# Kernel tuning notes

Measured on AMD Instinct MI355X. Metric: run time of the kernel, lower is better.

The kernel has to match this reference:

```python
import jax, jax.numpy as jnp
import numpy as np

N, E, F, HID, PC, HEADS = 100000, 1600000, 128, 128, 16, 4
RATIO = 0.8
NEG_SLOPE = 0.2
BIG_NEG = -1e9


def setup_inputs() -> dict:
    ks = jax.random.split(jax.random.key(0), 20)
    def g(k, shape, fan):
        return jax.random.normal(k, shape, jnp.float32) / np.float32(np.sqrt(fan))
    return {
        "x": jax.random.normal(ks[0], (N, F), jnp.float32),
        "edge_index": jax.random.randint(ks[1], (2, E), 0, N, dtype=jnp.int32),
        "edge_attr": jax.random.uniform(ks[2], (E, 1), dtype=jnp.float32),
        "W1": g(ks[3], (F, PC), F),
        "att_src1": g(ks[4], (HEADS, PC // HEADS), PC // HEADS),
        "att_dst1": g(ks[5], (HEADS, PC // HEADS), PC // HEADS),
        "We1": g(ks[6], (1, PC), 1),
        "att_edge1": g(ks[7], (HEADS, PC // HEADS), PC // HEADS),
        "b1": jnp.zeros((PC,), jnp.float32),
        "Wrel": g(ks[8], (PC, 1), PC),
        "brel": jnp.zeros((1,), jnp.float32),
        "Wroot": g(ks[9], (PC, 1), PC),
        "W2": g(ks[10], (PC, HID), PC),
        "att_src2": g(ks[11], (1, HID), HID),
        "att_dst2": g(ks[12], (1, HID), HID),
        "We2": g(ks[13], (1, HID), 1),
        "att_edge2": g(ks[14], (1, HID), HID),
        "b2": jnp.zeros((HID,), jnp.float32),
        "Wg": g(ks[15], (HID, 1), HID),
        "bg": jnp.zeros((1,), jnp.float32),
    }


def gat_conv(h_in, src, dst, e_attr, W, a_s, a_d, We, a_e, b, num_nodes, mask=None):
    """PyG GATConv (add_self_loops=False, eval-mode so dropout is identity)."""
    H, D = a_s.shape
    h = (h_in @ W).reshape(-1, H, D)                      # [N,H,D]
    al_s = jnp.einsum('nhd,hd->nh', h, a_s)               # alpha contribution of source
    al_d = jnp.einsum('nhd,hd->nh', h, a_d)               # alpha contribution of dest
    he = (e_attr @ We).reshape(-1, H, D)                  # [E,H,D] edge features
    al_e = jnp.einsum('ehd,hd->eh', he, a_e)              # [E,H]
    logits = jax.nn.leaky_relu(al_s[src] + al_d[dst] + al_e, NEG_SLOPE)  # [E,H]
    if mask is not None:
        logits = jnp.where(mask[:, None], logits, BIG_NEG)
    # segment softmax over incoming edges of each destination node
    m = jnp.maximum(jax.ops.segment_max(logits, dst, num_segments=num_nodes), BIG_NEG)
    num = jnp.exp(logits - m[dst])
    if mask is not None:
        num = jnp.where(mask[:, None], num, 0.0)
    den = jax.ops.segment_sum(num, dst, num_segments=num_nodes)
    coef = num / jnp.maximum(den[dst], 1e-16)             # [E,H]
    out = jax.ops.segment_sum(coef[:, :, None] * h[src], dst, num_segments=num_nodes)
    return out.reshape(num_nodes, H * D) + b


def _forward(x, edge_attr, W1, att_src1, att_dst1, We1, att_edge1, b1,
             Wrel, brel, Wroot, W2, att_src2, att_dst2, We2, att_edge2, b2,
             Wg, bg, edge_index):
    n = x.shape[0]
    src, dst = edge_index[0], edge_index[1]
    h1 = jax.nn.relu(gat_conv(x, src, dst, edge_attr, W1, att_src1, att_dst1, We1, att_edge1, b1, n))
    # --- SAGPooling: GraphConv score -> tanh -> top-k -> masked subgraph (n > node_threshold always) ---
    agg = jax.ops.segment_sum(h1[src], dst, num_segments=n)           # neighbor sum
    score = (agg @ Wrel + brel + h1 @ Wroot).reshape(-1)              # GraphConv(16 -> 1)
    k = int(np.ceil(RATIO * n))                                       # static
    vals, perm = jax.lax.top_k(score, k)
    new_idx = jnp.full((n,), -1, dtype=jnp.int32).at[perm].set(jnp.arange(k, dtype=jnp.int32))
    src_n, dst_n = new_idx[src], new_idx[dst]
    emask = (src_n >= 0) & (dst_n >= 0)                               # edges with both ends kept
    src2 = jnp.where(emask, src_n, 0)
    dst2 = jnp.where(emask, dst_n, 0)
    x2 = h1[perm] * jnp.tanh(vals)[:, None]                           # gate kept nodes
    h2 = jax.nn.relu(gat_conv(x2, src2, dst2, edge_attr, W2, att_src2, att_dst2, We2, att_edge2, b2, k, mask=emask))
    # --- AttentionalAggregation + MaxAggregation over the single graph (index = zeros) ---
    gate = jax.nn.softmax(h2 @ Wg + bg, axis=0)                       # [k,1]
    att = (gate * h2).sum(axis=0, keepdims=True)                      # [1,HID]
    mx = h2.max(axis=0, keepdims=True)                                # [1,HID]
    return jnp.concatenate([att, mx], axis=1)                         # [1,2*HID]


def reference(x, edge_index, edge_attr, W1, att_src1, att_dst1, We1, att_edge1, b1,
              Wrel, brel, Wroot, W2, att_src2, att_dst2, We2, att_edge2, b2, Wg, bg):
    return _forward(x, edge_attr, W1, att_src1, att_dst1, We1, att_edge1, b1,
                    Wrel, brel, Wroot, W2, att_src2, att_dst2, We2, att_edge2, b2,
                    Wg, bg, edge_index)
```

## Files before the change

kernel.cpp:

```cpp
#include <hip/hip_runtime.h>
#include <hip/hip_bf16.h>

#define Nn 100000
#define Ee 1600000
#define Kk 80000
#define NB ((Nn + 255) / 256)
#define NBK 196
#define CHK 8192
#define G2B 2048

typedef unsigned int uint;
typedef unsigned short ushort;

struct Scal {
    uint prefix, remaining;
    float c1[4];
    float c2;
};

__device__ __forceinline__ uint f2ord(float f) {
    uint b = __float_as_uint(f);
    return (b & 0x80000000u) ? ~b : (b | 0x80000000u);
}
__device__ __forceinline__ float lrelu(float v) { return v > 0.f ? v : 0.2f * v; }
__device__ __forceinline__ float2 bf2f2(uint u) {
    return make_float2(__uint_as_float(u << 16), __uint_as_float(u & 0xFFFF0000u));
}

__global__ __launch_bounds__(256) void initK(uint* bcnt, uint* hist, Scal* sc,
                                             const float* We1, const float* ae1,
                                             const float* We2, const float* ae2) {
    int i = blockIdx.x * 256 + threadIdx.x;
    if (i < NBK) bcnt[i] = 0u;
    if (i < 256) hist[i] = 0u;
    if (i == 0) {
        sc->prefix = 0u; sc->remaining = Kk;
        for (int h = 0; h < 4; h++) {
            float s = 0.f;
            for (int d = 0; d < 4; d++) s += We1[h * 4 + d] * ae1[h * 4 + d];
            sc->c1[h] = s;
        }
        float s2 = 0.f;
        for (int d = 0; d < 128; d++) s2 += We2[d] * ae2[d];
        sc->c2 = s2;
    }
}

__global__ __launch_bounds__(256) void nodeL1(const float* __restrict__ x,
                                              const float* __restrict__ W1,
                                              const float* __restrict__ as1,
                                              const float* __restrict__ ad1,
                                              float* __restrict__ hpre,
                                              float* __restrict__ alS1,
                                              float* __restrict__ alD1) {
    __shared__ float Ws[128 * 16];
    __shared__ float s_as[16], s_ad[16];
    for (int i = threadIdx.x; i < 2048; i += 256) Ws[i] = W1[i];
    if (threadIdx.x < 16) { s_as[threadIdx.x] = as1[threadIdx.x]; s_ad[threadIdx.x] = ad1[threadIdx.x]; }
    __syncthreads();
    int n = blockIdx.x * 256 + threadIdx.x;
    if (n >= Nn) return;
    float acc[16];
#pragma unroll
    for (int j = 0; j < 16; j++) acc[j] = 0.f;
    const float4* xr = (const float4*)(x + (size_t)n * 128);
    for (int t4 = 0; t4 < 32; t4++) {
        float4 xv = xr[t4];
#pragma unroll
        for (int j = 0; j < 16; j++) {
            acc[j] += xv.x * Ws[(t4 * 4 + 0) * 16 + j];
            acc[j] += xv.y * Ws[(t4 * 4 + 1) * 16 + j];
            acc[j] += xv.z * Ws[(t4 * 4 + 2) * 16 + j];
            acc[j] += xv.w * Ws[(t4 * 4 + 3) * 16 + j];
        }
    }
    float* hp = hpre + (size_t)n * 16;
#pragma unroll
    for (int j = 0; j < 16; j++) hp[j] = acc[j];
#pragma unroll
    for (int h = 0; h < 4; h++) {
        float s = 0.f, d = 0.f;
#pragma unroll
        for (int q = 0; q < 4; q++) {
            s += acc[h * 4 + q] * s_as[h * 4 + q];
            d += acc[h * 4 + q] * s_ad[h * 4 + q];
        }
        alS1[n * 4 + h] = s;
        alD1[n * 4 + h] = d;
    }
}

__global__ __launch_bounds__(256) void bucketCnt(const int* __restrict__ ei, uint* __restrict__ bcnt) {
    __shared__ uint h[NBK];
    if (threadIdx.x < NBK) h[threadIdx.x] = 0u;
    __syncthreads();
    for (int e = blockIdx.x * 256 + threadIdx.x; e < Ee; e += gridDim.x * 256)
        atomicAdd(&h[((uint)ei[Ee + e]) >> 9], 1u);
    __syncthreads();
    if (threadIdx.x < NBK && h[threadIdx.x]) atomicAdd(&bcnt[threadIdx.x], h[threadIdx.x]);
}

__global__ __launch_bounds__(256) void scanBk(const uint* __restrict__ bcnt, uint* __restrict__ boff,
                                              uint* __restrict__ gcur) {
    __shared__ uint s[256];
    int t = threadIdx.x;
    uint v = (t < NBK) ? bcnt[t] : 0u;
    s[t] = v;
    __syncthreads();
    for (int off = 1; off < 256; off <<= 1) {
        uint u = (t >= off) ? s[t - off] : 0u;
        __syncthreads();
        s[t] += u;
        __syncthreads();
    }
    if (t < NBK) { boff[t] = s[t] - v; gcur[t] = 0u; }
    if (t == 0) boff[NBK] = Ee;
}

__global__ __launch_bounds__(256) void binScat(const int* __restrict__ ei, const float* __restrict__ ea,
                                               const uint* __restrict__ boff, uint* __restrict__ gcur,
                                               uint2* __restrict__ bsE, ushort* __restrict__ bsD) {
    __shared__ uint h[NBK], base[NBK], h2[NBK];
    int t = threadIdx.x;
    if (t < NBK) h[t] = 0u;
    __syncthreads();
    int estart = blockIdx.x * CHK;
    int eend = min(Ee, estart + CHK);
    for (int e = estart + t; e < eend; e += 256)
        atomicAdd(&h[((uint)ei[Ee + e]) >> 9], 1u);
    __syncthreads();
    if (t < NBK) { base[t] = atomicAdd(&gcur[t], h[t]); h2[t] = 0u; }
    __syncthreads();
    for (int e = estart + t; e < eend; e += 256) {
        uint d = (uint)ei[Ee + e];
        uint b = d >> 9;
        uint r = atomicAdd(&h2[b], 1u);
        uint pos = boff[b] + base[b] + r;
        bsE[pos] = make_uint2((uint)ei[e], __float_as_uint(ea[e]));
        bsD[pos] = (ushort)(d & 511u);
    }
}

__global__ __launch_bounds__(256) void rankPlace(const uint* __restrict__ boff, const uint2* __restrict__ bsE,
                                                 const ushort* __restrict__ bsD,
                                                 uint2* __restrict__ csr_p8, uint* __restrict__ rowstart) {
    __shared__ uint ldeg[512];
    __shared__ uint lscan[512];
    __shared__ uint ps[256];
    int b = blockIdx.x, t = threadIdx.x;
    ldeg[t] = 0u; ldeg[t + 256] = 0u;
    __syncthreads();
    uint r0 = boff[b], r1 = boff[b + 1];
    for (uint i = r0 + t; i < r1; i += 256)
        atomicAdd(&ldeg[bsD[i]], 1u);
    __syncthreads();
    uint pv = ldeg[2 * t] + ldeg[2 * t + 1];
    ps[t] = pv;
    __syncthreads();
    for (int off = 1; off < 256; off <<= 1) {
        uint u = (t >= off) ? ps[t - off] : 0u;
        __syncthreads();
        ps[t] += u;
        __syncthreads();
    }
    uint pbase = ps[t] - pv;
    lscan[2 * t] = pbase;
    lscan[2 * t + 1] = pbase + ldeg[2 * t];
    __syncthreads();
    uint bb = boff[b];
    int nd = b * 512 + t;
    if (nd < Nn) rowstart[nd] = bb + lscan[t];
    nd = b * 512 + 256 + t;
    if (nd < Nn) rowstart[nd] = bb + lscan[256 + t];
    if (b == 0 && t == 0) rowstart[Nn] = Ee;
    ldeg[t] = 0u; ldeg[t + 256] = 0u;
    __syncthreads();
    for (uint i = r0 + t; i < r1; i += 256) {
        ushort dl = bsD[i];
        uint r = atomicAdd(&ldeg[dl], 1u);
        csr_p8[bb + lscan[dl] + r] = bsE[i];
    }
}

__global__ __launch_bounds__(256) void gather1f(const uint2* __restrict__ csr_p8,
                                                const uint* __restrict__ rowstart,
                                                const float* __restrict__ alS1, const float* __restrict__ alD1,
                                                const float* __restrict__ hpre, const Scal* __restrict__ scc,
                                                const float* __restrict__ b1, const float* __restrict__ Wrel,
                                                const float* __restrict__ Wroot,
                                                float* __restrict__ h1, float* __restrict__ p,
                                                float* __restrict__ q) {
    int tid = blockIdx.x * 256 + threadIdx.x;
    if (tid >= Nn * 4) return;
    int d = tid >> 2, h = tid & 3;
    uint r0 = rowstart[d], r1 = rowstart[d + 1];
    float ad = alD1[tid];
    float c1h = scc->c1[h];
    float den = 0.f;
    float4 acc = {0.f, 0.f, 0.f, 0.f};
#pragma unroll 8
    for (uint i = r0; i < r1; i++) {
        uint2 p8 = csr_p8[i];
        int s = (int)p8.x;
        float e = __expf(lrelu(alS1[s * 4 + h] + __uint_as_float(p8.y) * c1h + ad));
        float4 hv = *(const float4*)(hpre + (size_t)s * 16 + h * 4);
        den += e;
        acc.x += e * hv.x; acc.y += e * hv.y;
        acc.z += e * hv.z; acc.w += e * hv.w;
    }
    float inv = 1.f / fmaxf(den, 1e-16f);
    float4 o;
    o.x = fmaxf(acc.x * inv + b1[h * 4 + 0], 0.f);
    o.y = fmaxf(acc.y * inv + b1[h * 4 + 1], 0.f);
    o.z = fmaxf(acc.z * inv + b1[h * 4 + 2], 0.f);
    o.w = fmaxf(acc.w * inv + b1[h * 4 + 3], 0.f);
    *(float4*)(h1 + (size_t)d * 16 + h * 4) = o;
    float pp = o.x * Wrel[h * 4 + 0] + o.y * Wrel[h * 4 + 1] + o.z * Wrel[h * 4 + 2] + o.w * Wrel[h * 4 + 3];
    float qq = o.x * Wroot[h * 4 + 0] + o.y * Wroot[h * 4 + 1] + o.z * Wroot[h * 4 + 2] + o.w * Wroot[h * 4 + 3];
    pp += __shfl_xor(pp, 1); pp += __shfl_xor(pp, 2);
    qq += __shfl_xor(qq, 1); qq += __shfl_xor(qq, 2);
    if (h == 0) { p[d] = pp; q[d] = qq; }
}

__global__ __launch_bounds__(256) void scoreH(const uint2* __restrict__ csr_p8, const uint* __restrict__ rowstart,
                                              const float* __restrict__ p, const float* __restrict__ q,
                                              const float* __restrict__ brel,
                                              float* __restrict__ score, uint* __restrict__ dkey,
                                              uint* __restrict__ hist) {
    __shared__ uint lh[256];
    lh[threadIdx.x] = 0u;
    __syncthreads();
    int d = blockIdx.x * 256 + threadIdx.x;
    if (d < Nn) {
        uint r0 = rowstart[d], r1 = rowstart[d + 1];
        float s = brel[0] + q[d];
#pragma unroll 8
        for (uint i = r0; i < r1; i++) s += p[(int)csr_p8[i].x];
        score[d] = s;
        uint k = ~f2ord(s);
        dkey[d] = k;
        atomicAdd(&lh[k >> 24], 1u);
    }
    __syncthreads();
    if (lh[threadIdx.x]) atomicAdd(&hist[threadIdx.x], lh[threadIdx.x]);
}

__global__ __launch_bounds__(256) void histK(const uint* __restrict__ dkey, const Scal* __restrict__ sc,
                                             uint* __restrict__ hist, int shift) {
    __shared__ uint lh[256];
    lh[threadIdx.x] = 0u;
    __syncthreads();
    int i = blockIdx.x * 256 + threadIdx.x;
    if (i < Nn) {
        uint d = dkey[i];
        if ((d >> (shift + 8)) == sc->prefix) atomicAdd(&lh[(d >> shift) & 255u], 1u);
    }
    __syncthreads();
    if (lh[threadIdx.x]) atomicAdd(&hist[threadIdx.x], lh[threadIdx.x]);
}

__global__ __launch_bounds__(256) void selP(Scal* sc, uint* hist) {
    __shared__ uint s[256];
    int t = threadIdx.x;
    uint c = hist[t];
    s[t] = c;
    __syncthreads();
    for (int off = 1; off < 256; off <<= 1) {
        uint v = (t >= off) ? s[t - off] : 0u;
        __syncthreads();
        s[t] += v;
        __syncthreads();
    }
    uint rem = sc->remaining;
    uint cum = s[t];
    uint cumex = cum - c;
    if (cum >= rem && cumex < rem) {
        sc->remaining = rem - cumex;
        sc->prefix = (sc->prefix << 8) | (uint)t;
    }
    hist[t] = 0u;
}

__global__ __launch_bounds__(256) void eqCnt(const uint* __restrict__ dkey, const Scal* __restrict__ sc,
                                             uint* __restrict__ blkEq) {
    int i = blockIdx.x * 256 + threadIdx.x;
    uint ut = sc->prefix;
    bool eq = (i < Nn) && (dkey[i] == ut);
    __shared__ uint se[4];
    unsigned long long be = __ballot(eq);
    int lane = threadIdx.x & 63, w = threadIdx.x >> 6;
    if (lane == 0) se[w] = (uint)__popcll(be);
    __syncthreads();
    if (threadIdx.x == 0) blkEq[blockIdx.x] = se[0] + se[1] + se[2] + se[3];
}

__global__ __launch_bounds__(512) void prefE(const uint* __restrict__ blkEq, uint* __restrict__ eqPref) {
    __shared__ uint se[512];
    int t = threadIdx.x;
    uint e = (t < NB) ? blkEq[t] : 0u;
    se[t] = e;
    __syncthreads();
    for (int off = 1; off < 512; off <<= 1) {
        uint v1 = (t >= off) ? se[t - off] : 0u;
        __syncthreads();
        se[t] += v1;
        __syncthreads();
    }
    if (t < NB) eqPref[t] = se[t] - e;
}

__global__ __launch_bounds__(256) void keptK(const uint* __restrict__ dkey, const Scal* __restrict__ sc,
                                             const uint* __restrict__ eqPref, int* __restrict__ kept) {
    int i = blockIdx.x * 256 + threadIdx.x;
    uint ut = sc->prefix, needEq = sc->remaining;
    bool inr = i < Nn;
    uint d = inr ? dkey[i] : 0xFFFFFFFFu;
    bool isLt = inr && (d < ut);
    bool isEq = inr && (d == ut);
    __shared__ uint wcnt[4];
    unsigned long long mask = __ballot(isEq);
    int lane = threadIdx.x & 63, w = threadIdx.x >> 6;
    uint lanePre = (uint)__popcll(mask & ((1ull << lane) - 1ull));
    if (lane == 0) wcnt[w] = (uint)__popcll(mask);
    __syncthreads();
    uint wo = 0;
    for (int qq = 0; qq < 4; qq++) if (qq < w) wo += wcnt[qq];
    uint rank = eqPref[blockIdx.x] + wo + lanePre;
    if (inr) kept[i] = (isLt || (isEq && rank < needEq)) ? 1 : 0;
}

__global__ __launch_bounds__(256) void nodeL2(const float* __restrict__ h1, const float* __restrict__ score,
                                              const int* __restrict__ kept, const float* __restrict__ W2,
                                              const float* __restrict__ as2, const float* __restrict__ ad2,
                                              __hip_bfloat162* __restrict__ h2b, float* __restrict__ alS2k,
                                              float* __restrict__ alD2) {
    __shared__ float Ws[16 * 128];
    for (int i = threadIdx.x; i < 2048; i += 256) Ws[i] = W2[i];
    __syncthreads();
    int wid = (blockIdx.x * 256 + threadIdx.x) >> 6;
    int lane = threadIdx.x & 63;
    if (wid >= Nn) return;
    int n = wid;
    if (!kept[n]) { if (lane == 0) alS2k[n] = -1e30f; return; }
    float t = tanhf(score[n]);
    float x2[16];
    const float* hr = h1 + (size_t)n * 16;
#pragma unroll
    for (int j = 0; j < 16; j++) x2[j] = hr[j] * t;
    int d0 = 2 * lane, d1 = 2 * lane + 1;
    float a0 = 0.f, a1 = 0.f;
    const float2* Wv = (const float2*)Ws;
#pragma unroll
    for (int j = 0; j < 16; j++) {
        float2 wv = Wv[j * 64 + lane];
        a0 += x2[j] * wv.x;
        a1 += x2[j] * wv.y;
    }
    __hip_bfloat162 hb;
    hb.x = __float2bfloat16(a0);
    hb.y = __float2bfloat16(a1);
    h2b[(size_t)n * 64 + lane] = hb;
    float s = a0 * as2[d0] + a1 * as2[d1];
    float dd = a0 * ad2[d0] + a1 * ad2[d1];
#pragma unroll
    for (int off = 32; off; off >>= 1) { s += __shfl_xor(s, off); dd += __shfl_xor(dd, off); }
    if (lane == 0) { alS2k[n] = s; alD2[n] = dd; }
}

__global__ __launch_bounds__(256) void gather2g(const uint2* __restrict__ csr_p8,
                                                const uint* __restrict__ rowstart,
                                                const float* __restrict__ alS2k, const float* __restrict__ alD2,
                                                const Scal* __restrict__ scc,
                                                const __hip_bfloat162* __restrict__ h2b, const float* __restrict__ b2,
                                                const float* __restrict__ Wg, const float* __restrict__ bg,
                                                float* __restrict__ pacc, float* __restrict__ pmx,
                                                float* __restrict__ pden) {
    __shared__ float sAtt[4][16][8];
    __shared__ float sMx[4][16][8];
    __shared__ float sDen[4];
    int w = threadIdx.x >> 6, lane = threadIdx.x & 63;
    int g = lane >> 4, t = lane & 15;
    float4 b2a = ((const float4*)b2)[t * 2], b2b = ((const float4*)b2)[t * 2 + 1];
    float4 wga = ((const float4*)Wg)[t * 2], wgb = ((const float4*)Wg)[t * 2 + 1];
    float bg0 = bg[0];
    float c2 = scc->c2;
    const uint* h2u = (const uint*)h2b;
    float att[8], mx8[8], denP = 0.f;
#pragma unroll
    for (int j = 0; j < 8; j++) { att[j] = 0.f; mx8[j] = 0.f; }
    for (int n = blockIdx.x * 4 + w; n < Nn; n += G2B * 4) {
        float sk = alS2k[n];
        if (sk <= -1e29f) continue;
        float ad = alD2[n];
        uint r0 = rowstart[n];
        uint len = rowstart[n + 1] - r0;
        float den = 0.f;
        float acc[8];
#pragma unroll
        for (int d = 0; d < 8; d++) acc[d] = 0.f;
#pragma unroll 4
        for (uint base = 0; base < len; base += 4) {
            uint off = base + (uint)g;
            bool act = off < len;
            uint sidx = act ? (r0 + off) : (r0 + len - 1);
            uint2 p8 = csr_p8[sidx];
            int s = (int)p8.x;
            float pv = alS2k[s] + __uint_as_float(p8.y) * c2;
            pv = act ? pv : -1e30f;
            float c = __expf(lrelu(pv + ad));
            uint4 hv = *(const uint4*)(h2u + (size_t)s * 64 + t * 4);
            den += c;
            float2 f;
            f = bf2f2(hv.x); acc[0] += c * f.x; acc[1] += c * f.y;
            f = bf2f2(hv.y); acc[2] += c * f.x; acc[3] += c * f.y;
            f = bf2f2(hv.z); acc[4] += c * f.x; acc[5] += c * f.y;
            f = bf2f2(hv.w); acc[6] += c * f.x; acc[7] += c * f.y;
        }
#pragma unroll
        for (int d = 0; d < 8; d++) {
            acc[d] += __shfl_xor(acc[d], 16);
            acc[d] += __shfl_xor(acc[d], 32);
        }
        den += __shfl_xor(den, 16);
        den += __shfl_xor(den, 32);
        float inv = 1.f / fmaxf(den, 1e-16f);
        float o[8];
        o[0] = fmaxf(acc[0] * inv + b2a.x, 0.f);
        o[1] = fmaxf(acc[1] * inv + b2a.y, 0.f);
        o[2] = fmaxf(acc[2] * inv + b2a.z, 0.f);
        o[3] = fmaxf(acc[3] * inv + b2a.w, 0.f);
        o[4] = fmaxf(acc[4] * inv + b2b.x, 0.f);
        o[5] = fmaxf(acc[5] * inv + b2b.y, 0.f);
        o[6] = fmaxf(acc[6] * inv + b2b.z, 0.f);
        o[7] = fmaxf(acc[7] * inv + b2b.w, 0.f);
        float gp = o[0] * wga.x + o[1] * wga.y + o[2] * wga.z + o[3] * wga.w +
                   o[4] * wgb.x + o[5] * wgb.y + o[6] * wgb.z + o[7] * wgb.w;
#pragma unroll
        for (int off = 8; off; off >>= 1) gp += __shfl_xor(gp, off);
        float e = __expf(gp + bg0);
        denP += e;
#pragma unroll
        for (int j = 0; j < 8; j++) {
            att[j] += e * o[j];
            mx8[j] = fmaxf(mx8[j], o[j]);
        }
    }
    if (g == 0) {
#pragma unroll
        for (int j = 0; j < 8; j++) { sAtt[w][t][j] = att[j]; sMx[w][t][j] = mx8[j]; }
    }
    if (lane == 0) sDen[w] = denP;
    __syncthreads();
    int tid = threadIdx.x;
    if (tid < 128) {
        int tt = tid >> 3, j = tid & 7;
        float a = sAtt[0][tt][j] + sAtt[1][tt][j] + sAtt[2][tt][j] + sAtt[3][tt][j];
        float m = fmaxf(fmaxf(sMx[0][tt][j], sMx[1][tt][j]), fmaxf(sMx[2][tt][j], sMx[3][tt][j]));
        pacc[(size_t)blockIdx.x * 128 + tid] = a;
        pmx[(size_t)blockIdx.x * 128 + tid] = m;
    }
    if (tid == 0) pden[blockIdx.x] = sDen[0] + sDen[1] + sDen[2] + sDen[3];
}

__global__ __launch_bounds__(256) void gateOut(const float* __restrict__ pacc, const float* __restrict__ pmx,
                                               const float* __restrict__ pden, float* __restrict__ out) {
    __shared__ float r[256];
    __shared__ float rd[256];
    int b = blockIdx.x, tid = threadIdx.x;
    float a = 0.f, m = 0.f, dsum = 0.f;
    for (int i = tid; i < G2B; i += 256) {
        a += pacc[(size_t)i * 128 + b];
        m = fmaxf(m, pmx[(size_t)i * 128 + b]);
        dsum += pden[i];
    }
    r[tid] = a; rd[tid] = dsum;
    __syncthreads();
    for (int off = 128; off; off >>= 1) {
        if (tid < off) { r[tid] += r[tid + off]; rd[tid] += rd[tid + off]; }
        __syncthreads();
    }
    float asum = r[0], deng = rd[0];
    __syncthreads();
    r[tid] = m;
    __syncthreads();
    for (int off = 128; off; off >>= 1) {
        if (tid < off) r[tid] = fmaxf(r[tid], r[tid + off]);
        __syncthreads();
    }
    if (tid == 0) {
        out[b] = asum / deng;
        out[128 + b] = r[0];
    }
}

extern "C" void kernel_launch(void* const* d_in, const int* in_sizes, int n_in,
                              void* d_out, int out_size, void* d_ws, size_t ws_size,
                              hipStream_t stream) {
    const float* x = (const float*)d_in[0];
    const int* ei = (const int*)d_in[1];
    const float* ea = (const float*)d_in[2];
    const float* W1 = (const float*)d_in[3];
    const float* as1 = (const float*)d_in[4];
    const float* ad1 = (const float*)d_in[5];
    const float* We1 = (const float*)d_in[6];
    const float* ae1 = (const float*)d_in[7];
    const float* b1 = (const float*)d_in[8];
    const float* Wrel = (const float*)d_in[9];
    const float* brel = (const float*)d_in[10];
    const float* Wroot = (const float*)d_in[11];
    const float* W2 = (const float*)d_in[12];
    const float* as2 = (const float*)d_in[13];
    const float* ad2 = (const float*)d_in[14];
    const float* We2 = (const float*)d_in[15];
    const float* ae2 = (const float*)d_in[16];
    const float* b2 = (const float*)d_in[17];
    const float* Wg = (const float*)d_in[18];
    const float* bg = (const float*)d_in[19];
    float* out = (float*)d_out;

    float* base = (float*)d_ws;
    size_t o = 0;
    auto alloc = [&](size_t nf) { float* p2 = base + o; o += nf; return p2; };
    uint2* bsE = (uint2*)alloc((size_t)Ee * 2);
    ushort* bsD = (ushort*)alloc((size_t)Ee / 2);
    uint2* csr_p8 = (uint2*)alloc((size_t)Ee * 2);
    __hip_bfloat162* h2b = (__hip_bfloat162*)alloc((size_t)Nn * 64);
    float* hpre = alloc((size_t)Nn * 16);
    float* h1 = alloc((size_t)Nn * 16);
    float* pacc = alloc((size_t)G2B * 128);
    float* pmx = alloc((size_t)G2B * 128);
    float* pden = alloc(G2B);
    float* alS1 = alloc((size_t)Nn * 4);
    float* alD1 = alloc((size_t)Nn * 4);
    float* p = alloc(Nn);
    float* q = alloc(Nn);
    float* score = alloc(Nn);
    uint* dkey = (uint*)alloc(Nn);
    int* kept = (int*)alloc(Nn);
    float* alS2k = alloc(Nn);
    float* alD2 = alloc(Nn);
    uint* rowstart = (uint*)alloc(Nn + 1);
    uint* hist = (uint*)alloc(256);
    uint* blkEq = (uint*)alloc(NB);
    uint* eqPref = (uint*)alloc(NB);
    uint* bcnt = (uint*)alloc(NBK);
    uint* boff = (uint*)alloc(NBK + 1);
    uint* gcur = (uint*)alloc(NBK);
    Scal* sc = (Scal*)alloc(64);

    auto cdiv = [](long a, long b) { return (int)((a + b - 1) / b); };

    initK<<<NB, 256, 0, stream>>>(bcnt, hist, sc, We1, ae1, We2, ae2);
    nodeL1<<<NB, 256, 0, stream>>>(x, W1, as1, ad1, hpre, alS1, alD1);
    bucketCnt<<<512, 256, 0, stream>>>(ei, bcnt);
    scanBk<<<1, 256, 0, stream>>>(bcnt, boff, gcur);
    binScat<<<cdiv(Ee, CHK), 256, 0, stream>>>(ei, ea, boff, gcur, bsE, bsD);
    rankPlace<<<NBK, 256, 0, stream>>>(boff, bsE, bsD, csr_p8, rowstart);
    gather1f<<<cdiv((long)Nn * 4, 256), 256, 0, stream>>>(csr_p8, rowstart, alS1, alD1, hpre, sc,
                                                          b1, Wrel, Wroot, h1, p, q);
    scoreH<<<NB, 256, 0, stream>>>(csr_p8, rowstart, p, q, brel, score, dkey, hist);
    selP<<<1, 256, 0, stream>>>(sc, hist);
    for (int shift = 16; shift >= 0; shift -= 8) {
        histK<<<NB, 256, 0, stream>>>(dkey, sc, hist, shift);
        selP<<<1, 256, 0, stream>>>(sc, hist);
    }
    eqCnt<<<NB, 256, 0, stream>>>(dkey, sc, blkEq);
    prefE<<<1, 512, 0, stream>>>(blkEq, eqPref);
    keptK<<<NB, 256, 0, stream>>>(dkey, sc, eqPref, kept);
    nodeL2<<<cdiv(Nn, 4), 256, 0, stream>>>(h1, score, kept, W2, as2, ad2, h2b, alS2k, alD2);
    gather2g<<<G2B, 256, 0, stream>>>(csr_p8, rowstart, alS2k, alD2, sc,
                                      h2b, b2, Wg, bg, pacc, pmx, pden);
    gateOut<<<128, 256, 0, stream>>>(pacc, pmx, pden, out);
}
```

Before: 328.0 us.

## Store layer-1 node features as bf16 and use finer 256-node CSR buckets

The projected layer-1 node features are now written as packed bf16 instead of fp32, which halves the bytes fetched per edge in the gather1f aggregation. The CSR build is reorganised around 256-node buckets (391 of them) with smaller per-block edge chunks. This gives more blocks for binScat and rankPlace and lighter per-block local scans. The bf16 storage costs precision in the layer-1 aggregation, which feeds the top-k score selection and could change which nodes are kept.

Measured after the change: 335.4 us. +2.3%, slower.

```diff
diff --git a/kernel.cpp b/kernel.cpp
--- a/kernel.cpp
+++ b/kernel.cpp
@@ -5,8 +5,8 @@
 #define Ee 1600000
 #define Kk 80000
 #define NB ((Nn + 255) / 256)
-#define NBK 196
-#define CHK 8192
+#define NBK 391
+#define CHK 2048
 #define G2B 2048
 
 typedef unsigned int uint;
@@ -25,6 +25,12 @@
 __device__ __forceinline__ float lrelu(float v) { return v > 0.f ? v : 0.2f * v; }
 __device__ __forceinline__ float2 bf2f2(uint u) {
     return make_float2(__uint_as_float(u << 16), __uint_as_float(u & 0xFFFF0000u));
+}
+__device__ __forceinline__ uint f2bf2(float a, float b) {
+    __hip_bfloat162 h;
+    h.x = __float2bfloat16(a);
+    h.y = __float2bfloat16(b);
+    return *(uint*)&h;
 }
 
 __global__ __launch_bounds__(256) void initK(uint* bcnt, uint* hist, Scal* sc,
@@ -50,7 +56,7 @@
                                               const float* __restrict__ W1,
                                               const float* __restrict__ as1,
                                               const float* __restrict__ ad1,
-                                              float* __restrict__ hpre,
+                                              uint* __restrict__ hpreB,
                                               float* __restrict__ alS1,
                                               float* __restrict__ alD1) {
     __shared__ float Ws[128 * 16];
@@ -74,9 +80,12 @@
             acc[j] += xv.w * Ws[(t4 * 4 + 3) * 16 + j];
         }
     }
-    float* hp = hpre + (size_t)n * 16;
-#pragma unroll
-    for (int j = 0; j < 16; j++) hp[j] = acc[j];
+    uint h8[8];
+#pragma unroll
+    for (int j = 0; j < 8; j++) h8[j] = f2bf2(acc[2 * j], acc[2 * j + 1]);
+    uint4* hp = (uint4*)(hpreB + (size_t)n * 8);
+    hp[0] = make_uint4(h8[0], h8[1], h8[2], h8[3]);
+    hp[1] = make_uint4(h8[4], h8[5], h8[6], h8[7]);
 #pragma unroll
     for (int h = 0; h < 4; h++) {
         float s = 0.f, d = 0.f;
@@ -92,22 +101,23 @@
 
 __global__ __launch_bounds__(256) void bucketCnt(const int* __restrict__ ei, uint* __restrict__ bcnt) {
     __shared__ uint h[NBK];
-    if (threadIdx.x < NBK) h[threadIdx.x] = 0u;
+    for (int k = threadIdx.x; k < NBK; k += 256) h[k] = 0u;
     __syncthreads();
     for (int e = blockIdx.x * 256 + threadIdx.x; e < Ee; e += gridDim.x * 256)
-        atomicAdd(&h[((uint)ei[Ee + e]) >> 9], 1u);
-    __syncthreads();
-    if (threadIdx.x < NBK && h[threadIdx.x]) atomicAdd(&bcnt[threadIdx.x], h[threadIdx.x]);
-}
-
-__global__ __launch_bounds__(256) void scanBk(const uint* __restrict__ bcnt, uint* __restrict__ boff,
+        atomicAdd(&h[((uint)ei[Ee + e]) >> 8], 1u);
+    __syncthreads();
+    for (int k = threadIdx.x; k < NBK; k += 256)
+        if (h[k]) atomicAdd(&bcnt[k], h[k]);
+}
+
+__global__ __launch_bounds__(512) void scanBk(const uint* __restrict__ bcnt, uint* __restrict__ boff,
                                               uint* __restrict__ gcur) {
-    __shared__ uint s[256];
+    __shared__ uint s[512];
     int t = threadIdx.x;
     uint v = (t < NBK) ? bcnt[t] : 0u;
     s[t] = v;
     __syncthreads();
-    for (int off = 1; off < 256; off <<= 1) {
+    for (int off = 1; off < 512; off <<= 1) {
         uint u = (t >= off) ? s[t - off] : 0u;
         __syncthreads();
         s[t] += u;
@@ -122,58 +132,57 @@
                                                uint2* __restrict__ bsE, ushort* __restrict__ bsD) {
     __shared__ uint h[NBK], base[NBK], h2[NBK];
     int t = threadIdx.x;
-    if (t < NBK) h[t] = 0u;
+    for (int k = t; k < NBK; k += 256) h[k] = 0u;
     __syncthreads();
     int estart = blockIdx.x * CHK;
     int eend = min(Ee, estart + CHK);
     for (int e = estart + t; e < eend; e += 256)
-        atomicAdd(&h[((uint)ei[Ee + e]) >> 9], 1u);
-    __syncthreads();
-    if (t < NBK) { base[t] = atomicAdd(&gcur[t], h[t]); h2[t] = 0u; }
+        atomicAdd(&h[((uint)ei[Ee + e]) >> 8], 1u);
+    __syncthreads();
+    for (int k = t; k < NBK; k += 256) {
+        base[k] = h[k] ? atomicAdd(&gcur[k], h[k]) : 0u;
+        h2[k] = 0u;
+    }
     __syncthreads();
     for (int e = estart + t; e < eend; e += 256) {
         uint d = (uint)ei[Ee + e];
-        uint b = d >> 9;
+        uint b = d >> 8;
         uint r = atomicAdd(&h2[b], 1u);
         uint pos = boff[b] + base[b] + r;
         bsE[pos] = make_uint2((uint)ei[e], __float_as_uint(ea[e]));
-        bsD[pos] = (ushort)(d & 511u);
+        bsD[pos] = (ushort)(d & 255u);
     }
 }
 
 __global__ __launch_bounds__(256) void rankPlace(const uint* __restrict__ boff, const uint2* __restrict__ bsE,
                                                  const ushort* __restrict__ bsD,
                                                  uint2* __restrict__ csr_p8, uint* __restrict__ rowstart) {
-    __shared__ uint ldeg[512];
-    __shared__ uint lscan[512];
-    __shared__ uint ps[256];
+    __shared__ uint ldeg[256];
+    __shared__ uint lscan[256];
+    __shared__ uint s[256];
     int b = blockIdx.x, t = threadIdx.x;
-    ldeg[t] = 0u; ldeg[t + 256] = 0u;
+    ldeg[t] = 0u;
     __syncthreads();
     uint r0 = boff[b], r1 = boff[b + 1];
     for (uint i = r0 + t; i < r1; i += 256)
         atomicAdd(&ldeg[bsD[i]], 1u);
     __syncthreads();
-    uint pv = ldeg[2 * t] + ldeg[2 * t + 1];
-    ps[t] = pv;
+    uint v = ldeg[t];
+    s[t] = v;
     __syncthreads();
     for (int off = 1; off < 256; off <<= 1) {
-        uint u = (t >= off) ? ps[t - off] : 0u;
-        __syncthreads();
-        ps[t] += u;
-        __syncthreads();
-    }
-    uint pbase = ps[t] - pv;
-    lscan[2 * t] = pbase;
-    lscan[2 * t + 1] = pbase + ldeg[2 * t];
+        uint u = (t >= off) ? s[t - off] : 0u;
+        __syncthreads();
+        s[t] += u;
+        __syncthreads();
+    }
+    lscan[t] = s[t] - v;
     __syncthreads();
     uint bb = boff[b];
-    int nd = b * 512 + t;
+    int nd = b * 256 + t;
     if (nd < Nn) rowstart[nd] = bb + lscan[t];
-    nd = b * 512 + 256 + t;
-    if (nd < Nn) rowstart[nd] = bb + lscan[256 + t];
     if (b == 0 && t == 0) rowstart[Nn] = Ee;
-    ldeg[t] = 0u; ldeg[t + 256] = 0u;
+    ldeg[t] = 0u;
     __syncthreads();
     for (uint i = r0 + t; i < r1; i += 256) {
         ushort dl = bsD[i];
@@ -185,7 +194,7 @@
 __global__ __launch_bounds__(256) void gather1f(const uint2* __restrict__ csr_p8,
                                                 const uint* __restrict__ rowstart,
                                                 const float* __restrict__ alS1, const float* __restrict__ alD1,
-                                                const float* __restrict__ hpre, const Scal* __restrict__ scc,
+                                                const uint* __restrict__ hpreB, const Scal* __restrict__ scc,
                                                 const float* __restrict__ b1, const float* __restrict__ Wrel,
                                                 const float* __restrict__ Wroot,
                                                 float* __restrict__ h1, float* __restrict__ p,
@@ -203,10 +212,11 @@
         uint2 p8 = csr_p8[i];
         int s = (int)p8.x;
         float e = __expf(lrelu(alS1[s * 4 + h] + __uint_as_float(p8.y) * c1h + ad));
-        float4 hv = *(const float4*)(hpre + (size_t)s * 16 + h * 4);
+        uint2 hb = *(const uint2*)(hpreB + (size_t)s * 8 + h * 2);
+        float2 f0 = bf2f2(hb.x), f1 = bf2f2(hb.y);
         den += e;
-        acc.x += e * hv.x; acc.y += e * hv.y;
-        acc.z += e * hv.z; acc.w += e * hv.w;
+        acc.x += e * f0.x; acc.y += e * f0.y;
+        acc.z += e * f1.x; acc.w += e * f1.y;
     }
     float inv = 1.f / fmaxf(den, 1e-16f);
     float4 o;
@@ -525,7 +535,7 @@
     ushort* bsD = (ushort*)alloc((size_t)Ee / 2);
     uint2* csr_p8 = (uint2*)alloc((size_t)Ee * 2);
     __hip_bfloat162* h2b = (__hip_bfloat162*)alloc((size_t)Nn * 64);
-    float* hpre = alloc((size_t)Nn * 16);
+    uint* hpreB = (uint*)alloc((size_t)Nn * 8);
     float* h1 = alloc((size_t)Nn * 16);
     float* pacc = alloc((size_t)G2B * 128);
     float* pmx = alloc((size_t)G2B * 128);
@@ -551,12 +561,12 @@
     auto cdiv = [](long a, long b) { return (int)((a + b - 1) / b); };
 
     initK<<<NB, 256, 0, stream>>>(bcnt, hist, sc, We1, ae1, We2, ae2);
-    nodeL1<<<NB, 256, 0, stream>>>(x, W1, as1, ad1, hpre, alS1, alD1);
+    nodeL1<<<NB, 256, 0, stream>>>(x, W1, as1, ad1, hpreB, alS1, alD1);
     bucketCnt<<<512, 256, 0, stream>>>(ei, bcnt);
-    scanBk<<<1, 256, 0, stream>>>(bcnt, boff, gcur);
+    scanBk<<<1, 512, 0, stream>>>(bcnt, boff, gcur);
     binScat<<<cdiv(Ee, CHK), 256, 0, stream>>>(ei, ea, boff, gcur, bsE, bsD);
     rankPlace<<<NBK, 256, 0, stream>>>(boff, bsE, bsD, csr_p8, rowstart);
-    gather1f<<<cdiv((long)Nn * 4, 256), 256, 0, stream>>>(csr_p8, rowstart, alS1, alD1, hpre, sc,
+    gather1f<<<cdiv((long)Nn * 4, 256), 256, 0, stream>>>(csr_p8, rowstart, alS1, alD1, hpreB, sc,
                                                           b1, Wrel, Wroot, h1, p, q);
     scoreH<<<NB, 256, 0, stream>>>(csr_p8, rowstart, p, q, brel, score, dkey, hist);
     selP<<<1, 256, 0, stream>>>(sc, hist);
```
